# Performance work log

Hardware: AMD Instinct MI355X
Metric: run time of the kernel (lower is better)

Reference implementation:

```python
import jax, jax.numpy as jnp
import numpy as np

FILTERS = 512
DQK = FILTERS // 8  # 64


def setup_inputs() -> dict:
    key = jax.random.key(0)
    ks = jax.random.split(key, 7)
    B, H, W, C = 32, 32, 32, FILTERS
    x = jax.random.normal(ks[0], (B, H, W, C), dtype=jnp.float32)
    # 1x1 convs == per-pixel dense layers: weight [Cin, Cout], bias [Cout]
    def glorot(k, cin, cout):
        lim = np.sqrt(6.0 / (cin + cout)).astype(np.float32)
        return jax.random.uniform(k, (cin, cout), jnp.float32, -lim, lim)
    return {
        "x": x,
        "wq": glorot(ks[1], C, DQK), "bq": jnp.zeros((DQK,), jnp.float32),
        "wk": glorot(ks[2], C, DQK), "bk": jnp.zeros((DQK,), jnp.float32),
        "wv": glorot(ks[3], C, C),   "bv": jnp.zeros((C,), jnp.float32),
    }


def reference(x, wq, bq, wk, bk, wv, bv):
    B, H, W, C = x.shape
    N = H * W
    xf = x.reshape(B, N, C)                       # flatten spatial -> tokens
    q = xf @ wq + bq                              # [B, N, C//8]
    k = xf @ wk + bk                              # [B, N, C//8]
    v = xf @ wv + bv                              # [B, N, C]
    scale = 1.0 / jnp.sqrt(jnp.float32(C // 8))
    scores = jnp.einsum('bnd,bmd->bnm', q, k) * scale  # [B, N, N]
    probs = jax.nn.softmax(scores, axis=-1)
    attended = jnp.einsum('bnm,bmc->bnc', probs, v)    # [B, N, C]
    return attended.reshape(B, H, W, C) + x
```

## Files before the change

### kernel.cpp

```cpp
#include <hip/hip_runtime.h>
#include <stdint.h>

#define B_ 32
#define N_ 1024
#define C_ 512
#define D_ 64

typedef __attribute__((ext_vector_type(8))) __bf16 bf8;
typedef __attribute__((ext_vector_type(4))) float f32x4;

typedef const __attribute__((address_space(1))) void* gp_t;
typedef __attribute__((address_space(3))) void* lp_t;

__device__ inline void g2l16(const void* g, void* l) {
    __builtin_amdgcn_global_load_lds((gp_t)g, (lp_t)l, 16, 0, 0);
}

__device__ inline float b2f(unsigned short u) {
    return __uint_as_float(((unsigned)u) << 16);
}
__device__ inline unsigned short f2b(float f) {
    unsigned u = __float_as_uint(f);
    u += 0x7FFF + ((u >> 16) & 1);
    return (unsigned short)(u >> 16);
}

#define MFMA16(a, b, c) __builtin_amdgcn_mfma_f32_16x16x32_bf16((a), (b), (c), 0, 0, 0)

__global__ __launch_bounds__(256) void xcvt(const float* __restrict__ x,
                                            unsigned short* __restrict__ xb) {
    int i = blockIdx.x * 256 + threadIdx.x;
    float4 f = ((const float4*)x)[i];
    ushort4 o;
    o.x = f2b(f.x); o.y = f2b(f.y); o.z = f2b(f.z); o.w = f2b(f.w);
    ((ushort4*)xb)[i] = o;
}

__global__ __launch_bounds__(256) void wtrans(const float* __restrict__ w,
                                              unsigned short* __restrict__ wt,
                                              int cout) {
    int t = blockIdx.x * 256 + threadIdx.x;
    int co = t >> 9;
    int ci = t & 511;
    wt[t] = f2b(w[(size_t)ci * cout + co]);
}

__global__ __launch_bounds__(256) void qkv(
    const unsigned short* __restrict__ xb,
    const unsigned short* __restrict__ WT,
    const float* __restrict__ bq, const float* __restrict__ bk,
    const float* __restrict__ bv,
    unsigned short* __restrict__ q, unsigned short* __restrict__ k,
    unsigned short* __restrict__ vT)
{
    const int rb = blockIdx.x;
    const int cb = blockIdx.y;
    const int tid = threadIdx.x;
    const int lane = tid & 63;
    const int wave = tid >> 6;
    const int wm = wave >> 1, wn = wave & 1;
    const int lr = lane & 15;
    const int lk = lane >> 4;

    __shared__ unsigned short SM[16896];
    unsigned short* As = SM;
    unsigned short* Bs = SM + 8192;
    unsigned short* TB = SM;

    const int row0 = rb * 128;
    const int col0 = cb * 128;

    f32x4 zero4 = {0.f, 0.f, 0.f, 0.f};
    f32x4 acc[4][4];
    #pragma unroll
    for (int i = 0; i < 4; ++i)
        #pragma unroll
        for (int j = 0; j < 4; ++j) acc[i][j] = zero4;

    for (int kk = 0; kk < C_; kk += 64) {
        __syncthreads();
        #pragma unroll
        for (int i = 0; i < 4; ++i) {
            int f = wave * 4 + i;
            int t = f >> 1, kq = f & 1;
            g2l16(xb + (size_t)(row0 + t * 16 + lr) * C_ + kk + kq * 32 + lk * 8,
                  &As[f * 512]);
            g2l16(WT + (size_t)(col0 + t * 16 + lr) * C_ + kk + kq * 32 + lk * 8,
                  &Bs[f * 512]);
        }
        __syncthreads();
        #pragma unroll
        for (int kq = 0; kq < 2; ++kq) {
            bf8 a[4], bb[4];
            #pragma unroll
            for (int ti = 0; ti < 4; ++ti)
                a[ti] = *(const bf8*)&As[((wm * 4 + ti) * 2 + kq) * 512 + lane * 8];
            #pragma unroll
            for (int tj = 0; tj < 4; ++tj)
                bb[tj] = *(const bf8*)&Bs[((wn * 4 + tj) * 2 + kq) * 512 + lane * 8];
            #pragma unroll
            for (int ti = 0; ti < 4; ++ti)
                #pragma unroll
                for (int tj = 0; tj < 4; ++tj)
                    acc[ti][tj] = MFMA16(a[ti], bb[tj], acc[ti][tj]);
        }
    }

    if (cb == 0) {
        unsigned short* outp = (wn == 0) ? q : k;
        const float* bias = (wn == 0) ? bq : bk;
        #pragma unroll
        for (int ti = 0; ti < 4; ++ti)
            #pragma unroll
            for (int tj = 0; tj < 4; ++tj) {
                int col = tj * 16 + lr;
                float bi = bias[col];
                #pragma unroll
                for (int r = 0; r < 4; ++r) {
                    int row = row0 + wm * 64 + ti * 16 + lk * 4 + r;
                    outp[(size_t)row * D_ + col] = f2b(acc[ti][tj][r] + bi);
                }
            }
    } else {
        const int colv = (cb - 1) * 128;
        __syncthreads();
        #pragma unroll
        for (int ti = 0; ti < 4; ++ti)
            #pragma unroll
            for (int tj = 0; tj < 4; ++tj) {
                int c = wn * 64 + tj * 16 + lr;
                float bi = bv[colv + c];
                int tok = wm * 64 + ti * 16 + lk * 4;
                ushort4 o;
                o.x = f2b(acc[ti][tj][0] + bi);
                o.y = f2b(acc[ti][tj][1] + bi);
                o.z = f2b(acc[ti][tj][2] + bi);
                o.w = f2b(acc[ti][tj][3] + bi);
                *(ushort4*)&TB[c * 132 + tok] = o;
            }
        __syncthreads();
        const int b  = row0 >> 10;
        const int n0 = row0 & 1023;
        #pragma unroll
        for (int i = 0; i < 16; ++i) {
            int idx = tid + 256 * i;
            int c = idx >> 5, ch = idx & 31;
            ushort4 t4 = *(const ushort4*)&TB[c * 132 + ch * 4];
            *(ushort4*)&vT[((size_t)(b * C_ + colv + c)) * N_ + n0 + ch * 4] = t4;
        }
    }
}

#define SLD 1032
__global__ __launch_bounds__(256) void scores(
    const unsigned short* __restrict__ q,
    const unsigned short* __restrict__ k,
    unsigned short* __restrict__ P)
{
    const int qt = blockIdx.x, b = blockIdx.y;
    const int tid = threadIdx.x, lane = tid & 63, wave = tid >> 6;
    const int lr = lane & 15, lk = lane >> 4;
    __shared__ unsigned short S[16 * SLD];

    const int n0 = qt * 16;
    const unsigned short* qrow = q + (size_t)(b * N_ + n0 + lr) * D_ + lk * 8;
    bf8 qa0 = *(const bf8*)(qrow);
    bf8 qa1 = *(const bf8*)(qrow + 32);

    const int m0w = wave * 256;
    #pragma unroll 4
    for (int mt = 0; mt < 16; ++mt) {
        int m = m0w + mt * 16;
        const unsigned short* krow = k + (size_t)(b * N_ + m + lr) * D_ + lk * 8;
        bf8 kb0 = *(const bf8*)(krow);
        bf8 kb1 = *(const bf8*)(krow + 32);
        f32x4 s = {0.f, 0.f, 0.f, 0.f};
        s = MFMA16(qa0, kb0, s);
        s = MFMA16(qa1, kb1, s);
        #pragma unroll
        for (int r = 0; r < 4; ++r)
            S[(lk * 4 + r) * SLD + m + lr] = f2b(s[r] * 0.125f);
    }
    __syncthreads();

    #pragma unroll
    for (int rr4 = 0; rr4 < 4; ++rr4) {
        int rr = wave * 4 + rr4;
        float vals[16];
        float mx = -1e30f;
        #pragma unroll
        for (int j = 0; j < 16; ++j) {
            vals[j] = b2f(S[rr * SLD + j * 64 + lane]);
            mx = fmaxf(mx, vals[j]);
        }
        #pragma unroll
        for (int off = 32; off; off >>= 1) mx = fmaxf(mx, __shfl_xor(mx, off));
        float sum = 0.f;
        #pragma unroll
        for (int j = 0; j < 16; ++j) { vals[j] = __expf(vals[j] - mx); sum += vals[j]; }
        #pragma unroll
        for (int off = 32; off; off >>= 1) sum += __shfl_xor(sum, off);
        float inv = 1.f / sum;
        unsigned short* pp = P + (size_t)(b * N_ + n0 + rr) * N_;
        #pragma unroll
        for (int j = 0; j < 16; ++j) pp[j * 64 + lane] = f2b(vals[j] * inv);
    }
}

__global__ __launch_bounds__(256) void pv(
    const unsigned short* __restrict__ P,
    const unsigned short* __restrict__ vT,
    const float* __restrict__ x,
    float* __restrict__ out)
{
    const int m0 = blockIdx.x * 128, c0 = blockIdx.y * 128, b = blockIdx.z;
    const int tid = threadIdx.x, lane = tid & 63, wave = tid >> 6;
    const int wm = wave >> 1, wn = wave & 1;
    const int lr = lane & 15, lk = lane >> 4;

    __shared__ unsigned short As[128 * 64];
    __shared__ unsigned short Bs[128 * 64];

    f32x4 zero4 = {0.f, 0.f, 0.f, 0.f};
    f32x4 acc[4][4];
    #pragma unroll
    for (int i = 0; i < 4; ++i)
        #pragma unroll
        for (int j = 0; j < 4; ++j) acc[i][j] = zero4;

    const unsigned short* Pb = P  + (size_t)b * N_ * N_;
    const unsigned short* Vb = vT + (size_t)b * C_ * N_;

    for (int kk = 0; kk < N_; kk += 64) {
        __syncthreads();
        #pragma unroll
        for (int i = 0; i < 4; ++i) {
            int f = wave * 4 + i;
            int t = f >> 1, kq = f & 1;
            g2l16(Pb + (size_t)(m0 + t * 16 + lr) * N_ + kk + kq * 32 + lk * 8,
                  &As[f * 512]);
            g2l16(Vb + (size_t)(c0 + t * 16 + lr) * N_ + kk + kq * 32 + lk * 8,
                  &Bs[f * 512]);
        }
        __syncthreads();
        #pragma unroll
        for (int kq = 0; kq < 2; ++kq) {
            bf8 a[4], bb[4];
            #pragma unroll
            for (int ti = 0; ti < 4; ++ti)
                a[ti] = *(const bf8*)&As[((wm * 4 + ti) * 2 + kq) * 512 + lane * 8];
            #pragma unroll
            for (int tj = 0; tj < 4; ++tj)
                bb[tj] = *(const bf8*)&Bs[((wn * 4 + tj) * 2 + kq) * 512 + lane * 8];
            #pragma unroll
            for (int ti = 0; ti < 4; ++ti)
                #pragma unroll
                for (int tj = 0; tj < 4; ++tj)
                    acc[ti][tj] = MFMA16(a[ti], bb[tj], acc[ti][tj]);
        }
    }

    #pragma unroll
    for (int ti = 0; ti < 4; ++ti)
        #pragma unroll
        for (int tj = 0; tj < 4; ++tj) {
            int col = c0 + wn * 64 + tj * 16 + lr;
            #pragma unroll
            for (int r = 0; r < 4; ++r) {
                int row = m0 + wm * 64 + ti * 16 + lk * 4 + r;
                size_t idx = (size_t)(b * N_ + row) * C_ + col;
                out[idx] = acc[ti][tj][r] + x[idx];
            }
        }
}

extern "C" void kernel_launch(void* const* d_in, const int* in_sizes, int n_in,
                              void* d_out, int out_size, void* d_ws, size_t ws_size,
                              hipStream_t stream) {
    (void)in_sizes; (void)n_in; (void)out_size; (void)ws_size;
    const float* xf = (const float*)d_in[0];
    const float* wq = (const float*)d_in[1];
    const float* bq = (const float*)d_in[2];
    const float* wk = (const float*)d_in[3];
    const float* bk = (const float*)d_in[4];
    const float* wv = (const float*)d_in[5];
    const float* bv = (const float*)d_in[6];
    float* out = (float*)d_out;

    char* ws = (char*)d_ws;
    unsigned short* qb  = (unsigned short*)(ws);
    unsigned short* kb  = (unsigned short*)(ws + 4194304);
    unsigned short* vTb = (unsigned short*)(ws + 8388608);
    unsigned short* WT  = (unsigned short*)(ws + 41943040);
    unsigned short* xb  = (unsigned short*)(ws + 42598400);
    unsigned short* Pb  = (unsigned short*)(ws + 41943040);

    xcvt<<<16384, 256, 0, stream>>>(xf, xb);
    wtrans<<<128, 256, 0, stream>>>(wq, WT, 64);
    wtrans<<<128, 256, 0, stream>>>(wk, WT + 64 * 512, 64);
    wtrans<<<1024, 256, 0, stream>>>(wv, WT + 128 * 512, 512);
    qkv<<<dim3(256, 5), 256, 0, stream>>>(xb, WT, bq, bk, bv, qb, kb, vTb);
    scores<<<dim3(64, 32), 256, 0, stream>>>(qb, kb, Pb);
    pv<<<dim3(8, 4, 32), 256, 0, stream>>>(Pb, vTb, xf, out);
}
```

Measured before the change: 294.5 us.

## Double-buffer LDS tiles in qkv and pv GEMMs and merge weight transposes

The qkv and pv GEMM kernels now use two LDS buffers. Each iteration loads the current tile's fragments into registers, issues the async global-to-LDS load for the next tile, then runs the MFMAs, so global latency overlaps compute and one barrier per iteration is dropped. The three weight-transpose launches are merged into one kernel that picks its source by output row. LDS per block doubles, which may lower occupancy, and register use rises because both k-halves are held at once.

```diff
diff --git a/kernel.cpp b/kernel.cpp
--- a/kernel.cpp
+++ b/kernel.cpp
@@ -36,13 +36,19 @@
     ((ushort4*)xb)[i] = o;
 }
 
-__global__ __launch_bounds__(256) void wtrans(const float* __restrict__ w,
-                                              unsigned short* __restrict__ wt,
-                                              int cout) {
+__global__ __launch_bounds__(256) void wtrans_all(
+    const float* __restrict__ wq, const float* __restrict__ wk,
+    const float* __restrict__ wv, unsigned short* __restrict__ wt)
+{
     int t = blockIdx.x * 256 + threadIdx.x;
     int co = t >> 9;
     int ci = t & 511;
-    wt[t] = f2b(w[(size_t)ci * cout + co]);
+    const float* src;
+    int col, cout;
+    if (co < 64)       { src = wq; col = co;       cout = 64;  }
+    else if (co < 128) { src = wk; col = co - 64;  cout = 64;  }
+    else               { src = wv; col = co - 128; cout = 512; }
+    wt[t] = f2b(src[(size_t)ci * cout + col]);
 }
 
 __global__ __launch_bounds__(256) void qkv(
@@ -62,9 +68,7 @@
     const int lr = lane & 15;
     const int lk = lane >> 4;
 
-    __shared__ unsigned short SM[16896];
-    unsigned short* As = SM;
-    unsigned short* Bs = SM + 8192;
+    __shared__ unsigned short SM[32768];
     unsigned short* TB = SM;
 
     const int row0 = rb * 128;
@@ -77,8 +81,9 @@
         #pragma unroll
         for (int j = 0; j < 4; ++j) acc[i][j] = zero4;
 
-    for (int kk = 0; kk < C_; kk += 64) {
-        __syncthreads();
+    auto stage = [&](int buf, int kk) {
+        unsigned short* As = SM + buf * 8192;
+        unsigned short* Bs = SM + 16384 + buf * 8192;
         #pragma unroll
         for (int i = 0; i < 4; ++i) {
             int f = wave * 4 + i;
@@ -88,7 +93,39 @@
             g2l16(WT + (size_t)(col0 + t * 16 + lr) * C_ + kk + kq * 32 + lk * 8,
                   &Bs[f * 512]);
         }
+    };
+
+    stage(0, 0);
+    __syncthreads();
+    int cur = 0;
+    for (int kk = 64; kk < C_; kk += 64) {
+        const unsigned short* As = SM + cur * 8192;
+        const unsigned short* Bs = SM + 16384 + cur * 8192;
+        bf8 a[2][4], bb[2][4];
+        #pragma unroll
+        for (int kq = 0; kq < 2; ++kq) {
+            #pragma unroll
+            for (int ti = 0; ti < 4; ++ti)
+                a[kq][ti] = *(const bf8*)&As[((wm * 4 + ti) * 2 + kq) * 512 + lane * 8];
+            #pragma unroll
+            for (int tj = 0; tj < 4; ++tj)
+                bb[kq][tj] = *(const bf8*)&Bs[((wn * 4 + tj) * 2 + kq) * 512 + lane * 8];
+        }
+        __builtin_amdgcn_sched_barrier(0);
+        stage(cur ^ 1, kk);
+        #pragma unroll
+        for (int kq = 0; kq < 2; ++kq)
+            #pragma unroll
+            for (int ti = 0; ti < 4; ++ti)
+                #pragma unroll
+                for (int tj = 0; tj < 4; ++tj)
+                    acc[ti][tj] = MFMA16(a[kq][ti], bb[kq][tj], acc[ti][tj]);
         __syncthreads();
+        cur ^= 1;
+    }
+    {
+        const unsigned short* As = SM + cur * 8192;
+        const unsigned short* Bs = SM + 16384 + cur * 8192;
         #pragma unroll
         for (int kq = 0; kq < 2; ++kq) {
             bf8 a[4], bb[4];
@@ -218,8 +255,8 @@
     const int wm = wave >> 1, wn = wave & 1;
     const int lr = lane & 15, lk = lane >> 4;
 
-    __shared__ unsigned short As[128 * 64];
-    __shared__ unsigned short Bs[128 * 64];
+    __shared__ unsigned short As[2][8192];
+    __shared__ unsigned short Bs[2][8192];
 
     f32x4 zero4 = {0.f, 0.f, 0.f, 0.f};
     f32x4 acc[4][4];
@@ -231,27 +268,54 @@
     const unsigned short* Pb = P  + (size_t)b * N_ * N_;
     const unsigned short* Vb = vT + (size_t)b * C_ * N_;
 
-    for (int kk = 0; kk < N_; kk += 64) {
-        __syncthreads();
+    auto stage = [&](int buf, int kk) {
         #pragma unroll
         for (int i = 0; i < 4; ++i) {
             int f = wave * 4 + i;
             int t = f >> 1, kq = f & 1;
             g2l16(Pb + (size_t)(m0 + t * 16 + lr) * N_ + kk + kq * 32 + lk * 8,
-                  &As[f * 512]);
+                  &As[buf][f * 512]);
             g2l16(Vb + (size_t)(c0 + t * 16 + lr) * N_ + kk + kq * 32 + lk * 8,
-                  &Bs[f * 512]);
-        }
+                  &Bs[buf][f * 512]);
+        }
+    };
+
+    stage(0, 0);
+    __syncthreads();
+    int cur = 0;
+    for (int kk = 64; kk < N_; kk += 64) {
+        bf8 a[2][4], bb[2][4];
+        #pragma unroll
+        for (int kq = 0; kq < 2; ++kq) {
+            #pragma unroll
+            for (int ti = 0; ti < 4; ++ti)
+                a[kq][ti] = *(const bf8*)&As[cur][((wm * 4 + ti) * 2 + kq) * 512 + lane * 8];
+            #pragma unroll
+            for (int tj = 0; tj < 4; ++tj)
+                bb[kq][tj] = *(const bf8*)&Bs[cur][((wn * 4 + tj) * 2 + kq) * 512 + lane * 8];
+        }
+        __builtin_amdgcn_sched_barrier(0);
+        stage(cur ^ 1, kk);
+        #pragma unroll
+        for (int kq = 0; kq < 2; ++kq)
+            #pragma unroll
+            for (int ti = 0; ti < 4; ++ti)
+                #pragma unroll
+                for (int tj = 0; tj < 4; ++tj)
+                    acc[ti][tj] = MFMA16(a[kq][ti], bb[kq][tj], acc[ti][tj]);
         __syncthreads();
+        cur ^= 1;
+    }
+    {
         #pragma unroll
         for (int kq = 0; kq < 2; ++kq) {
             bf8 a[4], bb[4];
             #pragma unroll
             for (int ti = 0; ti < 4; ++ti)
-                a[ti] = *(const bf8*)&As[((wm * 4 + ti) * 2 + kq) * 512 + lane * 8];
+                a[ti] = *(const bf8*)&As[cur][((wm * 4 + ti) * 2 + kq) * 512 + lane * 8];
             #pragma unroll
             for (int tj = 0; tj < 4; ++tj)
-                bb[tj] = *(const bf8*)&Bs[((wn * 4 + tj) * 2 + kq) * 512 + lane * 8];
+                bb[tj] = *(const bf8*)&Bs[cur][((wn * 4 + tj) * 2 + kq) * 512 + lane * 8];
             #pragma unroll
             for (int ti = 0; ti < 4; ++ti)
                 #pragma unroll
@@ -296,9 +360,7 @@
     unsigned short* Pb  = (unsigned short*)(ws + 41943040);
 
     xcvt<<<16384, 256, 0, stream>>>(xf, xb);
-    wtrans<<<128, 256, 0, stream>>>(wq, WT, 64);
-    wtrans<<<128, 256, 0, stream>>>(wk, WT + 64 * 512, 64);
-    wtrans<<<1024, 256, 0, stream>>>(wv, WT + 128 * 512, 512);
+    wtrans_all<<<1280, 256, 0, stream>>>(wq, wk, wv, WT);
     qkv<<<dim3(256, 5), 256, 0, stream>>>(xb, WT, bq, bk, bv, qb, kb, vTb);
     scores<<<dim3(64, 32), 256, 0, stream>>>(qb, kb, Pb);
     pv<<<dim3(8, 4, 32), 256, 0, stream>>>(Pb, vTb, xf, out);
```

Result: faster. 288.0 us (-2.2%).
